# Kernel optimization log

Hardware: AMD Instinct MI355X
Metric: run time of the kernel (lower is better)

The kernel has to match this reference:

```python
import jax, jax.numpy as jnp
import numpy as np
import math

H = 16
D_MODEL = 1024
D_K = D_MODEL // H
B = 4
S = 2048


def setup_inputs() -> dict:
    key = jax.random.key(0)
    ks = jax.random.split(key, 11)
    s_in = 1.0 / math.sqrt(D_MODEL)
    inp = {
        "query": jax.random.normal(ks[0], (B, S, D_MODEL), dtype=jnp.float32),
        "key_": jax.random.normal(ks[1], (B, S, D_MODEL), dtype=jnp.float32),
        "value": jax.random.normal(ks[2], (B, S, D_MODEL), dtype=jnp.float32),
        # stacked per-head projection weights: [h, d_model, d_k]
        "Wq": jax.random.uniform(ks[3], (H, D_MODEL, D_K), jnp.float32, -s_in, s_in),
        "bq": jax.random.uniform(ks[4], (H, D_K), jnp.float32, -s_in, s_in),
        "Wk": jax.random.uniform(ks[5], (H, D_MODEL, D_K), jnp.float32, -s_in, s_in),
        "bk": jax.random.uniform(ks[6], (H, D_K), jnp.float32, -s_in, s_in),
        "Wv": jax.random.uniform(ks[7], (H, D_MODEL, D_K), jnp.float32, -s_in, s_in),
        "bv": jax.random.uniform(ks[8], (H, D_K), jnp.float32, -s_in, s_in),
        "Wo": jax.random.uniform(ks[9], (D_MODEL, D_MODEL), jnp.float32, -s_in, s_in),
        "bo": jax.random.uniform(ks[10], (D_MODEL,), jnp.float32, -s_in, s_in),
    }
    return inp


def reference(query, key_, value, Wq, bq, Wk, bk, Wv, bv, Wo, bo):
    # Per-head projections, batched over heads: [b,s,m] x [h,m,k] -> [b,h,s,k]
    q = jnp.einsum("bsm,hmk->bhsk", query, Wq) + bq[None, :, None, :]
    k = jnp.einsum("bsm,hmk->bhsk", key_, Wk) + bk[None, :, None, :]
    v = jnp.einsum("bsm,hmk->bhsk", value, Wv) + bv[None, :, None, :]
    # scores: q @ k^T -> [b,h,Sq,Sk]
    scores = jnp.einsum("bhqk,bhsk->bhqs", q, k) / jnp.sqrt(jnp.float32(D_K))
    # NOTE: original code softmaxes over dim=1 of the per-head [N,Sq,Sk]
    # tensor, i.e. the QUERY axis (axis=2 here). Mask has no effect
    # (masked_fill result is discarded in the source), so it is omitted.
    attn = jax.nn.softmax(scores, axis=2)
    ctx = jnp.einsum("bhqs,bhsk->bhqk", attn, v)  # [b,h,Sq,d_k]
    # concat heads along last dim (head-major order matches torch.cat)
    ctx = jnp.transpose(ctx, (0, 2, 1, 3)).reshape(B, S, D_MODEL)
    out = ctx @ Wo.T + bo  # final_W; dropout = identity (eval mode)
    return out
```

## Files before the change

kernel.cpp:

```cpp
#include <hip/hip_runtime.h>


#define DEV __device__ __forceinline__

typedef __bf16 bf16x8 __attribute__((ext_vector_type(8)));
typedef float  f32x4  __attribute__((ext_vector_type(4)));

DEV unsigned short f2bf(float f) {
    __bf16 h = (__bf16)f;
    return __builtin_bit_cast(unsigned short, h);
}

DEV bf16x8 ldfrag(const unsigned short* p) {
    return *reinterpret_cast<const bf16x8*>(p);
}

DEV void cvt8_store(unsigned short* dst, float4 a, float4 b) {
    bf16x8 v;
    v[0]=(__bf16)a.x; v[1]=(__bf16)a.y; v[2]=(__bf16)a.z; v[3]=(__bf16)a.w;
    v[4]=(__bf16)b.x; v[5]=(__bf16)b.y; v[6]=(__bf16)b.z; v[7]=(__bf16)b.w;
    *reinterpret_cast<bf16x8*>(dst) = v;
}

#define MFMA(a,b,c) __builtin_amdgcn_mfma_f32_16x16x32_bf16((a),(b),(c),0,0,0)

__global__ __launch_bounds__(256) void wprep(const float* __restrict__ Wq,
                                             const float* __restrict__ Wk,
                                             const float* __restrict__ Wv,
                                             const float* __restrict__ Wo,
                                             unsigned short* __restrict__ Wt,
                                             unsigned short* __restrict__ Wot) {
    int idx = blockIdx.x * 256 + threadIdx.x;
    int which = blockIdx.y;
    if (which == 3) { Wot[idx] = f2bf(Wo[idx]); return; }
    const float* W = (which == 0) ? Wq : (which == 1) ? Wk : Wv;
    int n = idx >> 10, m = idx & 1023;
    int h = n >> 6, k = n & 63;
    Wt[(size_t)which * 1048576 + idx] = f2bf(W[h * 65536 + m * 64 + k]);
}

__global__ __launch_bounds__(256) void proj_gemm(
        const float* __restrict__ Xq, const float* __restrict__ Xk,
        const float* __restrict__ Xv, const unsigned short* __restrict__ Wt,
        const float* __restrict__ bq, const float* __restrict__ bk,
        const float* __restrict__ bv,
        unsigned short* __restrict__ Qh, unsigned short* __restrict__ Kh,
        unsigned short* __restrict__ Vt) {
    const int tid = threadIdx.x;
    const int bm = blockIdx.x, bn = blockIdx.y, z = blockIdx.z;
    const float* X = (z == 0) ? Xq : (z == 1) ? Xk : Xv;
    const unsigned short* Bt = Wt + (size_t)z * 1048576;
    const float* bias = (z == 0) ? bq : (z == 1) ? bk : bv;

    __shared__ __align__(16) unsigned short As[128 * 40];
    __shared__ __align__(16) unsigned short Bs[128 * 40];

    const int lane = tid & 63, wid = tid >> 6;
    const int l16 = lane & 15, quad = lane >> 4;
    const int wm = wid & 1, wn = wid >> 1;

    f32x4 acc[4][4] = {};

    for (int kt = 0; kt < 32; ++kt) {
        __syncthreads();
        const int k0 = kt * 32;
#pragma unroll
        for (int i = 0; i < 2; ++i) {
            int seg = tid + i * 256;
            int row = seg >> 2, s4 = seg & 3;
            const float* gp = X + (size_t)(bm * 128 + row) * 1024 + k0 + s4 * 8;
            float4 f0 = *(const float4*)gp;
            float4 f1 = *(const float4*)(gp + 4);
            cvt8_store(&As[row * 40 + s4 * 8], f0, f1);
            const unsigned short* bp = Bt + (size_t)(bn * 128 + row) * 1024 + k0 + s4 * 8;
            *(uint4*)&Bs[row * 40 + s4 * 8] = *(const uint4*)bp;
        }
        __syncthreads();
        bf16x8 af[4], bfr[4];
#pragma unroll
        for (int mi = 0; mi < 4; ++mi)
            af[mi] = ldfrag(&As[(wm * 64 + mi * 16 + l16) * 40 + quad * 8]);
#pragma unroll
        for (int ni = 0; ni < 4; ++ni)
            bfr[ni] = ldfrag(&Bs[(wn * 64 + ni * 16 + l16) * 40 + quad * 8]);
#pragma unroll
        for (int mi = 0; mi < 4; ++mi)
#pragma unroll
            for (int ni = 0; ni < 4; ++ni)
                acc[mi][ni] = MFMA(af[mi], bfr[ni], acc[mi][ni]);
    }

#pragma unroll
    for (int mi = 0; mi < 4; ++mi)
#pragma unroll
        for (int ni = 0; ni < 4; ++ni)
#pragma unroll
            for (int r = 0; r < 4; ++r) {
                int row = bm * 128 + wm * 64 + mi * 16 + quad * 4 + r;
                int col = bn * 128 + wn * 64 + ni * 16 + l16;
                float v = acc[mi][ni][r] + bias[col];
                int b = row >> 11, s = row & 2047;
                int h = col >> 6, k = col & 63;
                unsigned short o = f2bf(v);
                if (z == 2) {
                    Vt[(size_t)((b * 16 + h) * 64 + k) * 2048 + s] = o;
                } else {
                    unsigned short* O = (z == 0) ? Qh : Kh;
                    O[(size_t)((b * 16 + h) * 2048 + s) * 64 + k] = o;
                }
            }
}

__global__ __launch_bounds__(256) void colsum(const unsigned short* __restrict__ Qh,
                                              const unsigned short* __restrict__ Kh,
                                              float* __restrict__ Dcol) {
    const int tid = threadIdx.x;
    const int st = blockIdx.x, bh = blockIdx.y;
    const unsigned short* Qb = Qh + (size_t)bh * 2048 * 64;
    const unsigned short* Kb = Kh + (size_t)bh * 2048 * 64;

    __shared__ __align__(16) unsigned short Ks[128 * 72];
    __shared__ __align__(16) unsigned short Qs[128 * 72];
    __shared__ float Dtmp[2][128];

    const int lane = tid & 63, wid = tid >> 6;
    const int l16 = lane & 15, quad = lane >> 4;
    const int wm = wid & 1, wn = wid >> 1;

#pragma unroll
    for (int i = 0; i < 4; ++i) {
        int seg = tid + i * 256;
        int row = seg >> 3, sc = seg & 7;
        *(uint4*)&Ks[row * 72 + sc * 8] =
            *(const uint4*)&Kb[(size_t)(st * 128 + row) * 64 + sc * 8];
    }

    float psum[4] = {0.f, 0.f, 0.f, 0.f};
    for (int q0 = 0; q0 < 2048; q0 += 128) {
        __syncthreads();
#pragma unroll
        for (int i = 0; i < 4; ++i) {
            int seg = tid + i * 256;
            int row = seg >> 3, sc = seg & 7;
            *(uint4*)&Qs[row * 72 + sc * 8] =
                *(const uint4*)&Qb[(size_t)(q0 + row) * 64 + sc * 8];
        }
        __syncthreads();
        f32x4 acc[4][4] = {};
#pragma unroll
        for (int ks = 0; ks < 2; ++ks) {
            bf16x8 af[4], bfr[4];
#pragma unroll
            for (int mi = 0; mi < 4; ++mi)
                af[mi] = ldfrag(&Qs[(wm * 64 + mi * 16 + l16) * 72 + ks * 32 + quad * 8]);
#pragma unroll
            for (int ni = 0; ni < 4; ++ni)
                bfr[ni] = ldfrag(&Ks[(wn * 64 + ni * 16 + l16) * 72 + ks * 32 + quad * 8]);
#pragma unroll
            for (int mi = 0; mi < 4; ++mi)
#pragma unroll
                for (int ni = 0; ni < 4; ++ni)
                    acc[mi][ni] = MFMA(af[mi], bfr[ni], acc[mi][ni]);
        }
#pragma unroll
        for (int ni = 0; ni < 4; ++ni) {
            float d = 0.f;
#pragma unroll
            for (int mi = 0; mi < 4; ++mi)
#pragma unroll
                for (int r = 0; r < 4; ++r)
                    d += __expf(acc[mi][ni][r] * 0.125f);
            psum[ni] += d;
        }
    }
#pragma unroll
    for (int ni = 0; ni < 4; ++ni) {
        float v = psum[ni];
        v += __shfl_xor(v, 16, 64);
        v += __shfl_xor(v, 32, 64);
        if (quad == 0) Dtmp[wm][wn * 64 + ni * 16 + l16] = v;
    }
    __syncthreads();
    if (tid < 128)
        Dcol[(size_t)bh * 2048 + st * 128 + tid] = Dtmp[0][tid] + Dtmp[1][tid];
}

__global__ __launch_bounds__(256) void attnpv(const unsigned short* __restrict__ Qh,
                                              const unsigned short* __restrict__ Kh,
                                              const unsigned short* __restrict__ Vtg,
                                              const float* __restrict__ Dcol,
                                              unsigned short* __restrict__ Ctx) {
    const int tid = threadIdx.x;
    const int qt = blockIdx.x, bh = blockIdx.y;
    const int b = bh >> 4, h = bh & 15;
    const unsigned short* Qb = Qh + (size_t)bh * 2048 * 64;
    const unsigned short* Kb = Kh + (size_t)bh * 2048 * 64;
    const unsigned short* Vb = Vtg + (size_t)bh * 64 * 2048;
    const float* Db = Dcol + (size_t)bh * 2048;

    __shared__ __align__(16) unsigned short Qs[128 * 72];
    __shared__ __align__(16) unsigned short Ks[64 * 72];
    __shared__ __align__(16) unsigned short Vs[64 * 72];
    __shared__ __align__(16) unsigned short Ps[128 * 72];
    __shared__ float Dinv[64];

    const int lane = tid & 63, wid = tid >> 6;
    const int l16 = lane & 15, quad = lane >> 4;
    const int wm = wid & 1, wn = wid >> 1;

#pragma unroll
    for (int i = 0; i < 4; ++i) {
        int seg = tid + i * 256;
        int row = seg >> 3, sc = seg & 7;
        *(uint4*)&Qs[row * 72 + sc * 8] =
            *(const uint4*)&Qb[(size_t)(qt * 128 + row) * 64 + sc * 8];
    }

    f32x4 cacc[2][4] = {};
    for (int s0 = 0; s0 < 2048; s0 += 64) {
        __syncthreads();
#pragma unroll
        for (int i = 0; i < 2; ++i) {
            int seg = tid + i * 256;
            int row = seg >> 3, sc = seg & 7;
            *(uint4*)&Ks[row * 72 + sc * 8] =
                *(const uint4*)&Kb[(size_t)(s0 + row) * 64 + sc * 8];
            *(uint4*)&Vs[row * 72 + sc * 8] =
                *(const uint4*)&Vb[(size_t)row * 2048 + s0 + sc * 8];
        }
        if (tid < 64) Dinv[tid] = 1.0f / Db[s0 + tid];
        __syncthreads();

        f32x4 sacc[4][2] = {};
#pragma unroll
        for (int ks = 0; ks < 2; ++ks) {
            bf16x8 af[4], bfr[2];
#pragma unroll
            for (int mi = 0; mi < 4; ++mi)
                af[mi] = ldfrag(&Qs[(wm * 64 + mi * 16 + l16) * 72 + ks * 32 + quad * 8]);
#pragma unroll
            for (int nj = 0; nj < 2; ++nj)
                bfr[nj] = ldfrag(&Ks[(wn * 32 + nj * 16 + l16) * 72 + ks * 32 + quad * 8]);
#pragma unroll
            for (int mi = 0; mi < 4; ++mi)
#pragma unroll
                for (int nj = 0; nj < 2; ++nj)
                    sacc[mi][nj] = MFMA(af[mi], bfr[nj], sacc[mi][nj]);
        }
#pragma unroll
        for (int mi = 0; mi < 4; ++mi)
#pragma unroll
            for (int nj = 0; nj < 2; ++nj) {
                int scol = wn * 32 + nj * 16 + l16;
                float dinv = Dinv[scol];
#pragma unroll
                for (int r = 0; r < 4; ++r) {
                    int qrow = wm * 64 + mi * 16 + quad * 4 + r;
                    Ps[qrow * 72 + scol] = f2bf(__expf(sacc[mi][nj][r] * 0.125f) * dinv);
                }
            }
        __syncthreads();

#pragma unroll
        for (int ks2 = 0; ks2 < 2; ++ks2) {
            bf16x8 pa[2], vbf[4];
#pragma unroll
            for (int mi = 0; mi < 2; ++mi)
                pa[mi] = ldfrag(&Ps[(wid * 32 + mi * 16 + l16) * 72 + ks2 * 32 + quad * 8]);
#pragma unroll
            for (int ni = 0; ni < 4; ++ni)
                vbf[ni] = ldfrag(&Vs[(ni * 16 + l16) * 72 + ks2 * 32 + quad * 8]);
#pragma unroll
            for (int mi = 0; mi < 2; ++mi)
#pragma unroll
                for (int ni = 0; ni < 4; ++ni)
                    cacc[mi][ni] = MFMA(pa[mi], vbf[ni], cacc[mi][ni]);
        }
    }

#pragma unroll
    for (int mi = 0; mi < 2; ++mi)
#pragma unroll
        for (int ni = 0; ni < 4; ++ni)
#pragma unroll
            for (int r = 0; r < 4; ++r) {
                int q = qt * 128 + wid * 32 + mi * 16 + quad * 4 + r;
                int dk = ni * 16 + l16;
                Ctx[(size_t)(b * 2048 + q) * 1024 + h * 64 + dk] = f2bf(cacc[mi][ni][r]);
            }
}

__global__ __launch_bounds__(256) void out_gemm(const unsigned short* __restrict__ A,
                                                const unsigned short* __restrict__ Bt,
                                                const float* __restrict__ bias,
                                                float* __restrict__ Out) {
    const int tid = threadIdx.x;
    const int bm = blockIdx.x, bn = blockIdx.y;

    __shared__ __align__(16) unsigned short As[128 * 40];
    __shared__ __align__(16) unsigned short Bs[128 * 40];

    const int lane = tid & 63, wid = tid >> 6;
    const int l16 = lane & 15, quad = lane >> 4;
    const int wm = wid & 1, wn = wid >> 1;

    f32x4 acc[4][4] = {};
    for (int kt = 0; kt < 32; ++kt) {
        __syncthreads();
        const int k0 = kt * 32;
#pragma unroll
        for (int i = 0; i < 2; ++i) {
            int seg = tid + i * 256;
            int row = seg >> 2, s4 = seg & 3;
            *(uint4*)&As[row * 40 + s4 * 8] =
                *(const uint4*)&A[(size_t)(bm * 128 + row) * 1024 + k0 + s4 * 8];
            *(uint4*)&Bs[row * 40 + s4 * 8] =
                *(const uint4*)&Bt[(size_t)(bn * 128 + row) * 1024 + k0 + s4 * 8];
        }
        __syncthreads();
        bf16x8 af[4], bfr[4];
#pragma unroll
        for (int mi = 0; mi < 4; ++mi)
            af[mi] = ldfrag(&As[(wm * 64 + mi * 16 + l16) * 40 + quad * 8]);
#pragma unroll
        for (int ni = 0; ni < 4; ++ni)
            bfr[ni] = ldfrag(&Bs[(wn * 64 + ni * 16 + l16) * 40 + quad * 8]);
#pragma unroll
        for (int mi = 0; mi < 4; ++mi)
#pragma unroll
            for (int ni = 0; ni < 4; ++ni)
                acc[mi][ni] = MFMA(af[mi], bfr[ni], acc[mi][ni]);
    }
#pragma unroll
    for (int mi = 0; mi < 4; ++mi)
#pragma unroll
        for (int ni = 0; ni < 4; ++ni)
#pragma unroll
            for (int r = 0; r < 4; ++r) {
                int row = bm * 128 + wm * 64 + mi * 16 + quad * 4 + r;
                int col = bn * 128 + wn * 64 + ni * 16 + l16;
                Out[(size_t)row * 1024 + col] = acc[mi][ni][r] + bias[col];
            }
}

extern "C" void kernel_launch(void* const* d_in, const int* in_sizes, int n_in,
                              void* d_out, int out_size, void* d_ws, size_t ws_size,
                              hipStream_t stream) {
    (void)in_sizes; (void)n_in; (void)out_size; (void)ws_size;
    const float* query = (const float*)d_in[0];
    const float* key_  = (const float*)d_in[1];
    const float* value = (const float*)d_in[2];
    const float* Wq    = (const float*)d_in[3];
    const float* bq    = (const float*)d_in[4];
    const float* Wk    = (const float*)d_in[5];
    const float* bk    = (const float*)d_in[6];
    const float* Wv    = (const float*)d_in[7];
    const float* bv    = (const float*)d_in[8];
    const float* Wo    = (const float*)d_in[9];
    const float* bo    = (const float*)d_in[10];
    float* Out = (float*)d_out;

    char* ws = (char*)d_ws;
    const size_t MB = 1024 * 1024;
    unsigned short* Wt   = (unsigned short*)(ws);
    unsigned short* Wot  = (unsigned short*)(ws + 6 * MB);
    unsigned short* Qh   = (unsigned short*)(ws + 8 * MB);
    unsigned short* Kh   = (unsigned short*)(ws + 24 * MB);
    unsigned short* Vt   = (unsigned short*)(ws + 40 * MB);
    unsigned short* Ctx  = (unsigned short*)(ws + 56 * MB);
    float* Dcol          = (float*)(ws + 72 * MB);

    wprep<<<dim3(4096, 4), dim3(256), 0, stream>>>(Wq, Wk, Wv, Wo, Wt, Wot);
    proj_gemm<<<dim3(64, 8, 3), dim3(256), 0, stream>>>(query, key_, value, Wt,
                                                        bq, bk, bv, Qh, Kh, Vt);
    colsum<<<dim3(16, 64), dim3(256), 0, stream>>>(Qh, Kh, Dcol);
    attnpv<<<dim3(16, 64), dim3(256), 0, stream>>>(Qh, Kh, Vt, Dcol, Ctx);
    out_gemm<<<dim3(64, 8), dim3(256), 0, stream>>>(Ctx, Wot, bo, Out);
}
```

Baseline: 507.8 us.

## Fold softmax scale into Q, prescale V by column sums, keep fragments in registers

Q is scaled by log2(e)/sqrt(d_k) in the projection epilogue, so both the column-sum pass and the attention pass can use a bare exp2 with no per-element multiply. A new vscale kernel divides V by the per-key softmax denominators ahead of time, which removes the reciprocal load and the per-element multiply from the attention inner loop. The loop-invariant K fragments in colsum and Q fragments in attnpv now live in registers instead of shared memory, cutting LDS traffic. In exchange there is one more kernel launch with a read-modify-write of V, extra bf16 rounding of the scaled V, and higher register pressure.

```diff
diff --git a/kernel.cpp b/kernel.cpp
--- a/kernel.cpp
+++ b/kernel.cpp
@@ -13,6 +13,14 @@
 
 DEV bf16x8 ldfrag(const unsigned short* p) {
     return *reinterpret_cast<const bf16x8*>(p);
+}
+
+DEV float fast_exp2(float x) {
+#if __has_builtin(__builtin_amdgcn_exp2f)
+    return __builtin_amdgcn_exp2f(x);
+#else
+    return exp2f(x);
+#endif
 }
 
 DEV void cvt8_store(unsigned short* dst, float4 a, float4 b) {
@@ -23,6 +31,8 @@
 }
 
 #define MFMA(a,b,c) __builtin_amdgcn_mfma_f32_16x16x32_bf16((a),(b),(c),0,0,0)
+
+#define QSCALE 0.18033688011112042f
 
 __global__ __launch_bounds__(256) void wprep(const float* __restrict__ Wq,
                                              const float* __restrict__ Wk,
@@ -99,6 +109,7 @@
                 int row = bm * 128 + wm * 64 + mi * 16 + quad * 4 + r;
                 int col = bn * 128 + wn * 64 + ni * 16 + l16;
                 float v = acc[mi][ni][r] + bias[col];
+                if (z == 0) v *= QSCALE;
                 int b = row >> 11, s = row & 2047;
                 int h = col >> 6, k = col & 63;
                 unsigned short o = f2bf(v);
@@ -119,7 +130,6 @@
     const unsigned short* Qb = Qh + (size_t)bh * 2048 * 64;
     const unsigned short* Kb = Kh + (size_t)bh * 2048 * 64;
 
-    __shared__ __align__(16) unsigned short Ks[128 * 72];
     __shared__ __align__(16) unsigned short Qs[128 * 72];
     __shared__ float Dtmp[2][128];
 
@@ -127,13 +137,13 @@
     const int l16 = lane & 15, quad = lane >> 4;
     const int wm = wid & 1, wn = wid >> 1;
 
-#pragma unroll
-    for (int i = 0; i < 4; ++i) {
-        int seg = tid + i * 256;
-        int row = seg >> 3, sc = seg & 7;
-        *(uint4*)&Ks[row * 72 + sc * 8] =
-            *(const uint4*)&Kb[(size_t)(st * 128 + row) * 64 + sc * 8];
-    }
+    bf16x8 bfr[2][4];
+#pragma unroll
+    for (int ks = 0; ks < 2; ++ks)
+#pragma unroll
+        for (int ni = 0; ni < 4; ++ni)
+            bfr[ks][ni] = ldfrag(&Kb[(size_t)(st * 128 + wn * 64 + ni * 16 + l16) * 64 +
+                                     ks * 32 + quad * 8]);
 
     float psum[4] = {0.f, 0.f, 0.f, 0.f};
     for (int q0 = 0; q0 < 2048; q0 += 128) {
@@ -149,18 +159,15 @@
         f32x4 acc[4][4] = {};
 #pragma unroll
         for (int ks = 0; ks < 2; ++ks) {
-            bf16x8 af[4], bfr[4];
+            bf16x8 af[4];
 #pragma unroll
             for (int mi = 0; mi < 4; ++mi)
                 af[mi] = ldfrag(&Qs[(wm * 64 + mi * 16 + l16) * 72 + ks * 32 + quad * 8]);
 #pragma unroll
-            for (int ni = 0; ni < 4; ++ni)
-                bfr[ni] = ldfrag(&Ks[(wn * 64 + ni * 16 + l16) * 72 + ks * 32 + quad * 8]);
-#pragma unroll
             for (int mi = 0; mi < 4; ++mi)
 #pragma unroll
                 for (int ni = 0; ni < 4; ++ni)
-                    acc[mi][ni] = MFMA(af[mi], bfr[ni], acc[mi][ni]);
+                    acc[mi][ni] = MFMA(af[mi], bfr[ks][ni], acc[mi][ni]);
         }
 #pragma unroll
         for (int ni = 0; ni < 4; ++ni) {
@@ -169,7 +176,7 @@
             for (int mi = 0; mi < 4; ++mi)
 #pragma unroll
                 for (int r = 0; r < 4; ++r)
-                    d += __expf(acc[mi][ni][r] * 0.125f);
+                    d += fast_exp2(acc[mi][ni][r]);
             psum[ni] += d;
         }
     }
@@ -185,36 +192,51 @@
         Dcol[(size_t)bh * 2048 + st * 128 + tid] = Dtmp[0][tid] + Dtmp[1][tid];
 }
 
+__global__ __launch_bounds__(256) void vscale(unsigned short* __restrict__ Vt,
+                                              const float* __restrict__ Dcol) {
+    const int k = blockIdx.x, bh = blockIdx.y, t = threadIdx.x;
+    size_t base = ((size_t)bh * 64 + k) * 2048 + t * 8;
+    bf16x8 v = *(const bf16x8*)&Vt[base];
+    float4 d0 = *(const float4*)&Dcol[bh * 2048 + t * 8];
+    float4 d1 = *(const float4*)&Dcol[bh * 2048 + t * 8 + 4];
+    bf16x8 o;
+    o[0] = (__bf16)((float)v[0] / d0.x);
+    o[1] = (__bf16)((float)v[1] / d0.y);
+    o[2] = (__bf16)((float)v[2] / d0.z);
+    o[3] = (__bf16)((float)v[3] / d0.w);
+    o[4] = (__bf16)((float)v[4] / d1.x);
+    o[5] = (__bf16)((float)v[5] / d1.y);
+    o[6] = (__bf16)((float)v[6] / d1.z);
+    o[7] = (__bf16)((float)v[7] / d1.w);
+    *(bf16x8*)&Vt[base] = o;
+}
+
 __global__ __launch_bounds__(256) void attnpv(const unsigned short* __restrict__ Qh,
                                               const unsigned short* __restrict__ Kh,
-                                              const unsigned short* __restrict__ Vtg,
-                                              const float* __restrict__ Dcol,
+                                              const unsigned short* __restrict__ Vn,
                                               unsigned short* __restrict__ Ctx) {
     const int tid = threadIdx.x;
     const int qt = blockIdx.x, bh = blockIdx.y;
     const int b = bh >> 4, h = bh & 15;
     const unsigned short* Qb = Qh + (size_t)bh * 2048 * 64;
     const unsigned short* Kb = Kh + (size_t)bh * 2048 * 64;
-    const unsigned short* Vb = Vtg + (size_t)bh * 64 * 2048;
-    const float* Db = Dcol + (size_t)bh * 2048;
-
-    __shared__ __align__(16) unsigned short Qs[128 * 72];
+    const unsigned short* Vb = Vn + (size_t)bh * 64 * 2048;
+
     __shared__ __align__(16) unsigned short Ks[64 * 72];
     __shared__ __align__(16) unsigned short Vs[64 * 72];
     __shared__ __align__(16) unsigned short Ps[128 * 72];
-    __shared__ float Dinv[64];
 
     const int lane = tid & 63, wid = tid >> 6;
     const int l16 = lane & 15, quad = lane >> 4;
     const int wm = wid & 1, wn = wid >> 1;
 
-#pragma unroll
-    for (int i = 0; i < 4; ++i) {
-        int seg = tid + i * 256;
-        int row = seg >> 3, sc = seg & 7;
-        *(uint4*)&Qs[row * 72 + sc * 8] =
-            *(const uint4*)&Qb[(size_t)(qt * 128 + row) * 64 + sc * 8];
-    }
+    bf16x8 af[2][4];
+#pragma unroll
+    for (int ks = 0; ks < 2; ++ks)
+#pragma unroll
+        for (int mi = 0; mi < 4; ++mi)
+            af[ks][mi] = ldfrag(&Qb[(size_t)(qt * 128 + wm * 64 + mi * 16 + l16) * 64 +
+                                    ks * 32 + quad * 8]);
 
     f32x4 cacc[2][4] = {};
     for (int s0 = 0; s0 < 2048; s0 += 64) {
@@ -228,16 +250,12 @@
             *(uint4*)&Vs[row * 72 + sc * 8] =
                 *(const uint4*)&Vb[(size_t)row * 2048 + s0 + sc * 8];
         }
-        if (tid < 64) Dinv[tid] = 1.0f / Db[s0 + tid];
         __syncthreads();
 
         f32x4 sacc[4][2] = {};
 #pragma unroll
         for (int ks = 0; ks < 2; ++ks) {
-            bf16x8 af[4], bfr[2];
-#pragma unroll
-            for (int mi = 0; mi < 4; ++mi)
-                af[mi] = ldfrag(&Qs[(wm * 64 + mi * 16 + l16) * 72 + ks * 32 + quad * 8]);
+            bf16x8 bfr[2];
 #pragma unroll
             for (int nj = 0; nj < 2; ++nj)
                 bfr[nj] = ldfrag(&Ks[(wn * 32 + nj * 16 + l16) * 72 + ks * 32 + quad * 8]);
@@ -245,18 +263,17 @@
             for (int mi = 0; mi < 4; ++mi)
 #pragma unroll
                 for (int nj = 0; nj < 2; ++nj)
-                    sacc[mi][nj] = MFMA(af[mi], bfr[nj], sacc[mi][nj]);
+                    sacc[mi][nj] = MFMA(af[ks][mi], bfr[nj], sacc[mi][nj]);
         }
 #pragma unroll
         for (int mi = 0; mi < 4; ++mi)
 #pragma unroll
             for (int nj = 0; nj < 2; ++nj) {
                 int scol = wn * 32 + nj * 16 + l16;
-                float dinv = Dinv[scol];
 #pragma unroll
                 for (int r = 0; r < 4; ++r) {
                     int qrow = wm * 64 + mi * 16 + quad * 4 + r;
-                    Ps[qrow * 72 + scol] = f2bf(__expf(sacc[mi][nj][r] * 0.125f) * dinv);
+                    Ps[qrow * 72 + scol] = f2bf(fast_exp2(sacc[mi][nj][r]));
                 }
             }
         __syncthreads();
@@ -374,6 +391,7 @@
     proj_gemm<<<dim3(64, 8, 3), dim3(256), 0, stream>>>(query, key_, value, Wt,
                                                         bq, bk, bv, Qh, Kh, Vt);
     colsum<<<dim3(16, 64), dim3(256), 0, stream>>>(Qh, Kh, Dcol);
-    attnpv<<<dim3(16, 64), dim3(256), 0, stream>>>(Qh, Kh, Vt, Dcol, Ctx);
+    vscale<<<dim3(64, 64), dim3(256), 0, stream>>>(Vt, Dcol);
+    attnpv<<<dim3(16, 64), dim3(256), 0, stream>>>(Qh, Kh, Vt, Ctx);
     out_gemm<<<dim3(64, 8), dim3(256), 0, stream>>>(Ctx, Wot, bo, Out);
 }
```

Measured after the change: 517.4 us. Within noise of the previous version (+1.9%).
